# Kernel tuning notes

Hardware: AMD Instinct MI355X
Metric: run time of the kernel (lower is better)

The kernel has to match this reference:

```python
import jax, jax.numpy as jnp
import numpy as np

N = 8192       # nodes
E = 262144     # edges (avg degree 32)
F_IN, H, L = 512, 256, 64


def setup_inputs() -> dict:
    key = jax.random.key(0)
    ks = jax.random.split(key, 8)
    features = jax.random.normal(ks[0], (N, F_IN), dtype=jnp.float32)
    src = jax.random.randint(ks[1], (E,), 0, N)
    dst = jax.random.randint(ks[2], (E,), 0, N)
    # nn.Linear weights are [out_feats, in_feats]; scale ~ kaiming-ish small init
    W1 = jax.random.normal(ks[3], (H, F_IN), dtype=jnp.float32) * (1.0 / np.sqrt(F_IN))
    b1 = jnp.zeros((H,), dtype=jnp.float32)
    W2 = jax.random.normal(ks[4], (L, H), dtype=jnp.float32) * (1.0 / np.sqrt(H))
    b2 = jnp.zeros((L,), dtype=jnp.float32)
    W3 = jax.random.normal(ks[5], (L, H), dtype=jnp.float32) * (1.0 / np.sqrt(H))
    b3 = jnp.zeros((L,), dtype=jnp.float32)
    return {"features": features, "src": src, "dst": dst,
            "W1": W1, "b1": b1, "W2": W2, "b2": b2, "W3": W3, "b3": b3}


def _gcn_agg(h, src, dst):
    # DGL copy_src + sum: gather source node features along edges, scatter-sum to dst
    return jax.ops.segment_sum(h[src], dst, num_segments=N)  # [N, d]


def reference(features, src, dst, W1, b1, W2, b2, W3, b3):
    # GCN layer 1: aggregate then linear + relu  (dropout=0 -> identity)
    agg1 = _gcn_agg(features, src, dst)                 # [N, F_IN]
    hidden = jax.nn.relu(agg1 @ W1.T + b1)              # [N, H]
    # GCN layers 2 & 3 share the aggregated hidden (linear activation)
    agg2 = _gcn_agg(hidden, src, dst)                   # [N, H]
    mu = agg2 @ W2.T + b2                               # [N, L]
    logvar = agg2 @ W3.T + b3                           # [N, L]
    # eval-mode reparameterize: z = mu
    z = mu
    # inner-product decoder with sigmoid
    adj = jax.nn.sigmoid(z @ z.T)                       # [N, N]
    return adj, mu, logvar
```

## Files before the change

kernel.cpp:

```cpp
#include <hip/hip_runtime.h>
#include <hip/hip_bf16.h>

#define N_NODES 8192
#define N_EDGES 262144

typedef __attribute__((ext_vector_type(8))) short short8v;
typedef __attribute__((ext_vector_type(4))) float float4v;

static __device__ __forceinline__ unsigned short f2bf(float f) {
    unsigned u = __float_as_uint(f);
    unsigned r = (u + 0x7FFF + ((u >> 16) & 1)) >> 16;
    return (unsigned short)r;
}
static __device__ __forceinline__ float bf2f(unsigned short h) {
    return __uint_as_float(((unsigned)h) << 16);
}
static __device__ __forceinline__ short8v ld_cvt8(const float* p) {
    float4 lo = *(const float4*)p;
    float4 hi = *(const float4*)(p + 4);
    short8v r;
    r[0] = (short)f2bf(lo.x); r[1] = (short)f2bf(lo.y); r[2] = (short)f2bf(lo.z); r[3] = (short)f2bf(lo.w);
    r[4] = (short)f2bf(hi.x); r[5] = (short)f2bf(hi.y); r[6] = (short)f2bf(hi.z); r[7] = (short)f2bf(hi.w);
    return r;
}


__global__ __launch_bounds__(256) void hist_prep_kernel(const int* __restrict__ dst, int* __restrict__ deg,
                                                        const float* __restrict__ W1, const float* __restrict__ W2,
                                                        const float* __restrict__ W3,
                                                        unsigned short* __restrict__ W1b,
                                                        unsigned short* __restrict__ W23b) {
    int b = blockIdx.x;
    if (b < 1024) {
        int e = b * 256 + threadIdx.x;
        atomicAdd(&deg[dst[e]], 1);
        return;
    }
    int i4 = (b - 1024) * 1024 + threadIdx.x * 4;
    const float* srcp;
    unsigned short* dstp;
    int off;
    if (i4 < 131072)      { srcp = W1; dstp = W1b;          off = i4; }
    else if (i4 < 147456) { srcp = W2; dstp = W23b;         off = i4 - 131072; }
    else                  { srcp = W3; dstp = W23b + 16384; off = i4 - 147456; }
    float4 v = *(const float4*)&srcp[off];
    ushort4 o = {f2bf(v.x), f2bf(v.y), f2bf(v.z), f2bf(v.w)};
    *(ushort4*)&dstp[off] = o;
}

__global__ __launch_bounds__(256) void scatter_kernel(const int* __restrict__ src, const int* __restrict__ dst,
                                                      int* __restrict__ cur, int* __restrict__ csr) {
    int e = blockIdx.x * 256 + threadIdx.x;
    int d = dst[e];
    int p = atomicAdd(&cur[d], 1);
    csr[p] = src[e];
}


__global__ __launch_bounds__(256) void gemm1_scan_kernel(const float* __restrict__ X,
                                                         const unsigned short* __restrict__ W1b,
                                                         unsigned short* __restrict__ Y1b,
                                                         const int* __restrict__ deg,
                                                         int* __restrict__ offs, int* __restrict__ cur) {
    if (blockIdx.x == 256) {
        if (blockIdx.y != 0) return;
        __shared__ int wsum[4];
        int t = threadIdx.x, lane = t & 63, w = t >> 6;
        int v[32];
        int s = 0;
        const int4* dp = (const int4*)&deg[t * 32];
#pragma unroll
        for (int i = 0; i < 8; i++) {
            int4 x = dp[i];
            v[4*i] = x.x; v[4*i+1] = x.y; v[4*i+2] = x.z; v[4*i+3] = x.w;
            s += x.x + x.y + x.z + x.w;
        }
        int incl = s;
#pragma unroll
        for (int d = 1; d < 64; d <<= 1) {
            int u = __shfl_up(incl, d);
            if (lane >= d) incl += u;
        }
        if (lane == 63) wsum[w] = incl;
        __syncthreads();
        int base = 0;
#pragma unroll
        for (int i = 0; i < 4; i++) if (i < w) base += wsum[i];
        int ex = base + incl - s;
        int4* op = (int4*)&offs[t * 32];
        int4* cp = (int4*)&cur[t * 32];
#pragma unroll
        for (int i = 0; i < 8; i++) {
            int4 o;
            o.x = ex; ex += v[4*i];
            o.y = ex; ex += v[4*i+1];
            o.z = ex; ex += v[4*i+2];
            o.w = ex; ex += v[4*i+3];
            op[i] = o; cp[i] = o;
        }
        if (t == 255) offs[N_NODES] = ex;
        return;
    }
    const int tid = threadIdx.x;
    const int lane = tid & 63;
    const int w = tid >> 6;
    const int r = lane & 15, q = lane >> 4;
    const int m0 = blockIdx.x * 32;
    const int n0 = blockIdx.y * 128 + w * 32;
    const float* Ap = &X[q * 8];
    const unsigned short* Bp = &W1b[q * 8];
    float4v acc[2][2] = {};
    short8v a[2], b[2], an[2], bn[2];
#pragma unroll
    for (int i = 0; i < 2; i++) a[i] = ld_cvt8(&Ap[(size_t)(m0 + i * 16 + r) * 512]);
#pragma unroll
    for (int j = 0; j < 2; j++) b[j] = *(const short8v*)&Bp[(size_t)(n0 + j * 16 + r) * 512];
    for (int k = 32; k < 512; k += 32) {
#pragma unroll
        for (int i = 0; i < 2; i++) an[i] = ld_cvt8(&Ap[(size_t)(m0 + i * 16 + r) * 512 + k]);
#pragma unroll
        for (int j = 0; j < 2; j++) bn[j] = *(const short8v*)&Bp[(size_t)(n0 + j * 16 + r) * 512 + k];
#pragma unroll
        for (int i = 0; i < 2; i++)
#pragma unroll
            for (int j = 0; j < 2; j++)
                acc[i][j] = __builtin_amdgcn_mfma_f32_16x16x32_bf16(a[i], b[j], acc[i][j], 0, 0, 0);
#pragma unroll
        for (int i = 0; i < 2; i++) a[i] = an[i];
#pragma unroll
        for (int j = 0; j < 2; j++) b[j] = bn[j];
    }
#pragma unroll
    for (int i = 0; i < 2; i++)
#pragma unroll
        for (int j = 0; j < 2; j++)
            acc[i][j] = __builtin_amdgcn_mfma_f32_16x16x32_bf16(a[i], b[j], acc[i][j], 0, 0, 0);
#pragma unroll
    for (int i = 0; i < 2; i++)
#pragma unroll
        for (int j = 0; j < 2; j++) {
            int col = n0 + j * 16 + r;
#pragma unroll
            for (int t = 0; t < 4; t++) {
                int row = m0 + i * 16 + q * 4 + t;
                Y1b[(size_t)row * 256 + col] = f2bf(acc[i][j][t]);
            }
        }
}


__global__ __launch_bounds__(256) void agg_gemm2_kernel(const unsigned short* __restrict__ Yb,
                                                        const int* __restrict__ offs,
                                                        const int* __restrict__ csr,
                                                        const float* __restrict__ bias,
                                                        const unsigned short* __restrict__ W23b,
                                                        unsigned short* __restrict__ Zb) {
    __shared__ unsigned short Hs[16][264];
    const int w = threadIdx.x >> 6, lane = threadIdx.x & 63;
    const int nb = blockIdx.x * 16;
    float4 bv = *(const float4*)&bias[lane * 4];
    for (int nn = 0; nn < 4; nn++) {
        int node = nb + w * 4 + nn;
        int s = offs[node], e = offs[node + 1];
        float4 acc0 = {0.f, 0.f, 0.f, 0.f}, acc1 = {0.f, 0.f, 0.f, 0.f};
        int i = s;
        for (; i + 3 < e; i += 4) {
            int u0 = csr[i], u1 = csr[i + 1], u2 = csr[i + 2], u3 = csr[i + 3];
            ushort4 v0 = *(const ushort4*)&Yb[(size_t)u0 * 256 + lane * 4];
            ushort4 v1 = *(const ushort4*)&Yb[(size_t)u1 * 256 + lane * 4];
            ushort4 v2 = *(const ushort4*)&Yb[(size_t)u2 * 256 + lane * 4];
            ushort4 v3 = *(const ushort4*)&Yb[(size_t)u3 * 256 + lane * 4];
            acc0.x += bf2f(v0.x) + bf2f(v1.x); acc1.x += bf2f(v2.x) + bf2f(v3.x);
            acc0.y += bf2f(v0.y) + bf2f(v1.y); acc1.y += bf2f(v2.y) + bf2f(v3.y);
            acc0.z += bf2f(v0.z) + bf2f(v1.z); acc1.z += bf2f(v2.z) + bf2f(v3.z);
            acc0.w += bf2f(v0.w) + bf2f(v1.w); acc1.w += bf2f(v2.w) + bf2f(v3.w);
        }
        for (; i < e; i++) {
            int u = csr[i];
            ushort4 v = *(const ushort4*)&Yb[(size_t)u * 256 + lane * 4];
            acc0.x += bf2f(v.x); acc0.y += bf2f(v.y); acc0.z += bf2f(v.z); acc0.w += bf2f(v.w);
        }
        ushort4 o;
        o.x = f2bf(fmaxf(acc0.x + acc1.x + bv.x, 0.f));
        o.y = f2bf(fmaxf(acc0.y + acc1.y + bv.y, 0.f));
        o.z = f2bf(fmaxf(acc0.z + acc1.z + bv.z, 0.f));
        o.w = f2bf(fmaxf(acc0.w + acc1.w + bv.w, 0.f));
        *(ushort4*)&Hs[w * 4 + nn][lane * 4] = o;
    }
    __syncthreads();
    const int r = lane & 15, q = lane >> 4;
    const int jn0 = w * 32;
    float4v acc[2] = {};
#pragma unroll
    for (int k = 0; k < 256; k += 32) {
        short8v a  = *(const short8v*)&Hs[r][k + q * 8];
        short8v b0 = *(const short8v*)&W23b[(size_t)(jn0 + r) * 256 + k + q * 8];
        short8v b1 = *(const short8v*)&W23b[(size_t)(jn0 + 16 + r) * 256 + k + q * 8];
        acc[0] = __builtin_amdgcn_mfma_f32_16x16x32_bf16(a, b0, acc[0], 0, 0, 0);
        acc[1] = __builtin_amdgcn_mfma_f32_16x16x32_bf16(a, b1, acc[1], 0, 0, 0);
    }
#pragma unroll
    for (int j = 0; j < 2; j++)
#pragma unroll
        for (int t = 0; t < 4; t++)
            Zb[(size_t)(nb + q * 4 + t) * 128 + jn0 + j * 16 + r] = f2bf(acc[j][t]);
}


__global__ __launch_bounds__(256) void agg_split_kernel(const unsigned short* __restrict__ Zb,
                                                        const int* __restrict__ offs,
                                                        const int* __restrict__ csr, const float* __restrict__ b2,
                                                        const float* __restrict__ b3, float* __restrict__ mu,
                                                        float* __restrict__ lv, unsigned short* __restrict__ zb) {
    int node = blockIdx.x * 4 + (threadIdx.x >> 6);
    int lane = threadIdx.x & 63;
    int s = offs[node], e = offs[node + 1];
    float2 acc0 = {0.f, 0.f}, acc1 = {0.f, 0.f};
    int i = s;
    for (; i + 3 < e; i += 4) {
        int u0 = csr[i], u1 = csr[i + 1], u2 = csr[i + 2], u3 = csr[i + 3];
        ushort2 v0 = *(const ushort2*)&Zb[(size_t)u0 * 128 + lane * 2];
        ushort2 v1 = *(const ushort2*)&Zb[(size_t)u1 * 128 + lane * 2];
        ushort2 v2 = *(const ushort2*)&Zb[(size_t)u2 * 128 + lane * 2];
        ushort2 v3 = *(const ushort2*)&Zb[(size_t)u3 * 128 + lane * 2];
        acc0.x += bf2f(v0.x) + bf2f(v1.x); acc1.x += bf2f(v2.x) + bf2f(v3.x);
        acc0.y += bf2f(v0.y) + bf2f(v1.y); acc1.y += bf2f(v2.y) + bf2f(v3.y);
    }
    for (; i < e; i++) {
        int u = csr[i];
        ushort2 v = *(const ushort2*)&Zb[(size_t)u * 128 + lane * 2];
        acc0.x += bf2f(v.x); acc0.y += bf2f(v.y);
    }
    float2 acc = {acc0.x + acc1.x, acc0.y + acc1.y};
    int col = lane * 2;
    if (col < 64) {
        acc.x += b2[col]; acc.y += b2[col + 1];
        *(float2*)&mu[(size_t)node * 64 + col] = acc;
        ushort2 q = {f2bf(acc.x), f2bf(acc.y)};
        *(ushort2*)&zb[(size_t)node * 64 + col] = q;
    } else {
        col -= 64;
        acc.x += b3[col]; acc.y += b3[col + 1];
        *(float2*)&lv[(size_t)node * 64 + col] = acc;
    }
}


__global__ __launch_bounds__(256) void adj_mfma_sym_kernel(const unsigned short* __restrict__ zb,
                                                           float* __restrict__ out) {
    const int bx = blockIdx.x, by = blockIdx.y;
    if (by > bx) return;
    const int tid = threadIdx.x;
    const int lane = tid & 63;
    const int wid = tid >> 6;
    const int waveM = wid >> 1, waveN = wid & 1;
    const int m_base = bx * 128 + waveM * 64;
    const int n_base = by * 128 + waveN * 64;
    const int r = lane & 15;
    const int q = lane >> 4;

    short8v a[4][2], b[4][2];
#pragma unroll
    for (int i = 0; i < 4; i++)
#pragma unroll
        for (int s = 0; s < 2; s++) {
            a[i][s] = *(const short8v*)&zb[(size_t)(m_base + i * 16 + r) * 64 + s * 32 + q * 8];
            b[i][s] = *(const short8v*)&zb[(size_t)(n_base + i * 16 + r) * 64 + s * 32 + q * 8];
        }

    float4v acc[4][4] = {};
#pragma unroll
    for (int s = 0; s < 2; s++)
#pragma unroll
        for (int i = 0; i < 4; i++)
#pragma unroll
            for (int j = 0; j < 4; j++)
                acc[i][j] = __builtin_amdgcn_mfma_f32_16x16x32_bf16(a[i][s], b[j][s], acc[i][j], 0, 0, 0);

    const bool mirror = (bx != by);
#pragma unroll
    for (int i = 0; i < 4; i++)
#pragma unroll
        for (int j = 0; j < 4; j++) {
            int col = n_base + j * 16 + r;
            float4 vv;
#pragma unroll
            for (int t = 0; t < 4; t++) {
                int row = m_base + i * 16 + q * 4 + t;
                float v = 1.0f / (1.0f + __expf(-acc[i][j][t]));
                out[(size_t)row * N_NODES + col] = v;
                ((float*)&vv)[t] = v;
            }
            if (mirror) {
                *(float4*)&out[(size_t)col * N_NODES + m_base + i * 16 + q * 4] = vv;
            }
        }
}


extern "C" void kernel_launch(void* const* d_in, const int* in_sizes, int n_in,
                              void* d_out, int out_size, void* d_ws, size_t ws_size,
                              hipStream_t stream) {
    const float* X   = (const float*)d_in[0];
    const int*   src = (const int*)d_in[1];
    const int*   dst = (const int*)d_in[2];
    const float* W1  = (const float*)d_in[3];
    const float* b1  = (const float*)d_in[4];
    const float* W2  = (const float*)d_in[5];
    const float* b2  = (const float*)d_in[6];
    const float* W3  = (const float*)d_in[7];
    const float* b3  = (const float*)d_in[8];

    float* out    = (float*)d_out;
    float* adj    = out;
    float* mu_out = out + (size_t)N_NODES * N_NODES;
    float* lv_out = mu_out + (size_t)N_NODES * 64;

    char* ws = (char*)d_ws;
    size_t off = 0;
    auto alloc = [&](size_t bytes) -> void* {
        void* p = ws + off;
        off += (bytes + 1023) & ~(size_t)1023;
        return p;
    };
    int* deg            = (int*)alloc(N_NODES * 4);
    int* cur            = (int*)alloc(N_NODES * 4);
    int* offs           = (int*)alloc((N_NODES + 1) * 4);
    int* csr            = (int*)alloc(N_EDGES * 4);
    unsigned short* W1b = (unsigned short*)alloc(256 * 512 * 2);
    unsigned short* W23b= (unsigned short*)alloc(128 * 256 * 2);
    unsigned short* Y1b = (unsigned short*)alloc((size_t)N_NODES * 256 * 2);
    unsigned short* Zb  = (unsigned short*)alloc((size_t)N_NODES * 128 * 2);
    unsigned short* zb  = (unsigned short*)alloc((size_t)N_NODES * 64 * 2);

    hipMemsetAsync(deg, 0, N_NODES * sizeof(int), stream);
    hist_prep_kernel<<<1184, 256, 0, stream>>>(dst, deg, W1, W2, W3, W1b, W23b);
    gemm1_scan_kernel<<<dim3(257, 2), 256, 0, stream>>>(X, W1b, Y1b, deg, offs, cur);
    scatter_kernel<<<N_EDGES / 256, 256, 0, stream>>>(src, dst, cur, csr);
    agg_gemm2_kernel<<<N_NODES / 16, 256, 0, stream>>>(Y1b, offs, csr, b1, W23b, Zb);
    agg_split_kernel<<<N_NODES / 4, 256, 0, stream>>>(Zb, offs, csr, b2, b3, mu_out, lv_out, zb);
    adj_mfma_sym_kernel<<<dim3(64, 64), 256, 0, stream>>>(zb, adj);
}
```

Baseline: 429.9 us.

## Fuse degree histogram with GEMM1, drop weight pre-conversion, widen aggregation blocks

```diff
diff --git a/kernel.cpp b/kernel.cpp
--- a/kernel.cpp
+++ b/kernel.cpp
@@ -25,27 +25,103 @@
 }
 
 
-__global__ __launch_bounds__(256) void hist_prep_kernel(const int* __restrict__ dst, int* __restrict__ deg,
-                                                        const float* __restrict__ W1, const float* __restrict__ W2,
-                                                        const float* __restrict__ W3,
-                                                        unsigned short* __restrict__ W1b,
-                                                        unsigned short* __restrict__ W23b) {
-    int b = blockIdx.x;
+__global__ __launch_bounds__(256) void hist_gemm1_kernel(const int* __restrict__ dst, int* __restrict__ deg,
+                                                         const float* __restrict__ X,
+                                                         const float* __restrict__ W1,
+                                                         unsigned short* __restrict__ Y1b) {
+    const int b = blockIdx.x;
     if (b < 1024) {
         int e = b * 256 + threadIdx.x;
         atomicAdd(&deg[dst[e]], 1);
         return;
     }
-    int i4 = (b - 1024) * 1024 + threadIdx.x * 4;
-    const float* srcp;
-    unsigned short* dstp;
-    int off;
-    if (i4 < 131072)      { srcp = W1; dstp = W1b;          off = i4; }
-    else if (i4 < 147456) { srcp = W2; dstp = W23b;         off = i4 - 131072; }
-    else                  { srcp = W3; dstp = W23b + 16384; off = i4 - 147456; }
-    float4 v = *(const float4*)&srcp[off];
-    ushort4 o = {f2bf(v.x), f2bf(v.y), f2bf(v.z), f2bf(v.w)};
-    *(ushort4*)&dstp[off] = o;
+    const int g = b - 1024;
+    const int bx = g & 255, by = g >> 8;
+    const int tid = threadIdx.x;
+    const int lane = tid & 63;
+    const int w = tid >> 6;
+    const int r = lane & 15, q = lane >> 4;
+    const int m0 = bx * 32;
+    const int n0 = by * 128 + w * 32;
+    const float* Ap = &X[q * 8];
+    const float* Bp = &W1[q * 8];
+    float4v acc[2][2] = {};
+    short8v a[2], bb[2], an[2], bn[2];
+#pragma unroll
+    for (int i = 0; i < 2; i++) a[i] = ld_cvt8(&Ap[(size_t)(m0 + i * 16 + r) * 512]);
+#pragma unroll
+    for (int j = 0; j < 2; j++) bb[j] = ld_cvt8(&Bp[(size_t)(n0 + j * 16 + r) * 512]);
+    for (int k = 32; k < 512; k += 32) {
+#pragma unroll
+        for (int i = 0; i < 2; i++) an[i] = ld_cvt8(&Ap[(size_t)(m0 + i * 16 + r) * 512 + k]);
+#pragma unroll
+        for (int j = 0; j < 2; j++) bn[j] = ld_cvt8(&Bp[(size_t)(n0 + j * 16 + r) * 512 + k]);
+#pragma unroll
+        for (int i = 0; i < 2; i++)
+#pragma unroll
+            for (int j = 0; j < 2; j++)
+                acc[i][j] = __builtin_amdgcn_mfma_f32_16x16x32_bf16(a[i], bb[j], acc[i][j], 0, 0, 0);
+#pragma unroll
+        for (int i = 0; i < 2; i++) a[i] = an[i];
+#pragma unroll
+        for (int j = 0; j < 2; j++) bb[j] = bn[j];
+    }
+#pragma unroll
+    for (int i = 0; i < 2; i++)
+#pragma unroll
+        for (int j = 0; j < 2; j++)
+            acc[i][j] = __builtin_amdgcn_mfma_f32_16x16x32_bf16(a[i], bb[j], acc[i][j], 0, 0, 0);
+#pragma unroll
+    for (int i = 0; i < 2; i++)
+#pragma unroll
+        for (int j = 0; j < 2; j++) {
+            int col = n0 + j * 16 + r;
+#pragma unroll
+            for (int t = 0; t < 4; t++) {
+                int row = m0 + i * 16 + q * 4 + t;
+                Y1b[(size_t)row * 256 + col] = f2bf(acc[i][j][t]);
+            }
+        }
+}
+
+
+__global__ __launch_bounds__(256) void scan_kernel(const int* __restrict__ deg, int* __restrict__ offs,
+                                                   int* __restrict__ cur) {
+    __shared__ int wsum[4];
+    int t = threadIdx.x, lane = t & 63, w = t >> 6;
+    int v[32];
+    int s = 0;
+    const int4* dp = (const int4*)&deg[t * 32];
+#pragma unroll
+    for (int i = 0; i < 8; i++) {
+        int4 x = dp[i];
+        v[4*i] = x.x; v[4*i+1] = x.y; v[4*i+2] = x.z; v[4*i+3] = x.w;
+        s += x.x + x.y + x.z + x.w;
+    }
+    int incl = s;
+#pragma unroll
+    for (int d = 1; d < 64; d <<= 1) {
+        int u = __shfl_up(incl, d);
+        if (lane >= d) incl += u;
+    }
+    if (lane == 63) wsum[w] = incl;
+    __syncthreads();
+    int base = 0;
+#pragma unroll
+    for (int i = 0; i < 4; i++) if (i < w) base += wsum[i];
+    int ex = base + incl - s;
+    int4* op = (int4*)&offs[t * 32];
+    int4* cp = (int4*)&cur[t * 32];
+#pragma unroll
+    for (int i = 0; i < 8; i++) {
+        int4 o;
+        o.x = ex; ex += v[4*i];
+        o.y = ex; ex += v[4*i+1];
+        o.z = ex; ex += v[4*i+2];
+        o.w = ex; ex += v[4*i+3];
+        op[i] = o; cp[i] = o;
+    }
+    if (t == 255) offs[N_NODES] = ex;
 }
 
 __global__ __launch_bounds__(256) void scatter_kernel(const int* __restrict__ src, const int* __restrict__ dst,
@@ -57,110 +133,18 @@
 }
 
 
-__global__ __launch_bounds__(256) void gemm1_scan_kernel(const float* __restrict__ X,
-                                                         const unsigned short* __restrict__ W1b,
-                                                         unsigned short* __restrict__ Y1b,
-                                                         const int* __restrict__ deg,
-                                                         int* __restrict__ offs, int* __restrict__ cur) {
-    if (blockIdx.x == 256) {
-        if (blockIdx.y != 0) return;
-        __shared__ int wsum[4];
-        int t = threadIdx.x, lane = t & 63, w = t >> 6;
-        int v[32];
-        int s = 0;
-        const int4* dp = (const int4*)&deg[t * 32];
-#pragma unroll
-        for (int i = 0; i < 8; i++) {
-            int4 x = dp[i];
-            v[4*i] = x.x; v[4*i+1] = x.y; v[4*i+2] = x.z; v[4*i+3] = x.w;
-            s += x.x + x.y + x.z + x.w;
-        }
-        int incl = s;
-#pragma unroll
-        for (int d = 1; d < 64; d <<= 1) {
-            int u = __shfl_up(incl, d);
-            if (lane >= d) incl += u;
-        }
-        if (lane == 63) wsum[w] = incl;
-        __syncthreads();
-        int base = 0;
-#pragma unroll
-        for (int i = 0; i < 4; i++) if (i < w) base += wsum[i];
-        int ex = base + incl - s;
-        int4* op = (int4*)&offs[t * 32];
-        int4* cp = (int4*)&cur[t * 32];
-#pragma unroll
-        for (int i = 0; i < 8; i++) {
-            int4 o;
-            o.x = ex; ex += v[4*i];
-            o.y = ex; ex += v[4*i+1];
-            o.z = ex; ex += v[4*i+2];
-            o.w = ex; ex += v[4*i+3];
-            op[i] = o; cp[i] = o;
-        }
-        if (t == 255) offs[N_NODES] = ex;
-        return;
-    }
-    const int tid = threadIdx.x;
-    const int lane = tid & 63;
-    const int w = tid >> 6;
-    const int r = lane & 15, q = lane >> 4;
-    const int m0 = blockIdx.x * 32;
-    const int n0 = blockIdx.y * 128 + w * 32;
-    const float* Ap = &X[q * 8];
-    const unsigned short* Bp = &W1b[q * 8];
-    float4v acc[2][2] = {};
-    short8v a[2], b[2], an[2], bn[2];
-#pragma unroll
-    for (int i = 0; i < 2; i++) a[i] = ld_cvt8(&Ap[(size_t)(m0 + i * 16 + r) * 512]);
-#pragma unroll
-    for (int j = 0; j < 2; j++) b[j] = *(const short8v*)&Bp[(size_t)(n0 + j * 16 + r) * 512];
-    for (int k = 32; k < 512; k += 32) {
-#pragma unroll
-        for (int i = 0; i < 2; i++) an[i] = ld_cvt8(&Ap[(size_t)(m0 + i * 16 + r) * 512 + k]);
-#pragma unroll
-        for (int j = 0; j < 2; j++) bn[j] = *(const short8v*)&Bp[(size_t)(n0 + j * 16 + r) * 512 + k];
-#pragma unroll
-        for (int i = 0; i < 2; i++)
-#pragma unroll
-            for (int j = 0; j < 2; j++)
-                acc[i][j] = __builtin_amdgcn_mfma_f32_16x16x32_bf16(a[i], b[j], acc[i][j], 0, 0, 0);
-#pragma unroll
-        for (int i = 0; i < 2; i++) a[i] = an[i];
-#pragma unroll
-        for (int j = 0; j < 2; j++) b[j] = bn[j];
-    }
-#pragma unroll
-    for (int i = 0; i < 2; i++)
-#pragma unroll
-        for (int j = 0; j < 2; j++)
-            acc[i][j] = __builtin_amdgcn_mfma_f32_16x16x32_bf16(a[i], b[j], acc[i][j], 0, 0, 0);
-#pragma unroll
-    for (int i = 0; i < 2; i++)
-#pragma unroll
-        for (int j = 0; j < 2; j++) {
-            int col = n0 + j * 16 + r;
-#pragma unroll
-            for (int t = 0; t < 4; t++) {
-                int row = m0 + i * 16 + q * 4 + t;
-                Y1b[(size_t)row * 256 + col] = f2bf(acc[i][j][t]);
-            }
-        }
-}
-
-
-__global__ __launch_bounds__(256) void agg_gemm2_kernel(const unsigned short* __restrict__ Yb,
-                                                        const int* __restrict__ offs,
-                                                        const int* __restrict__ csr,
-                                                        const float* __restrict__ bias,
-                                                        const unsigned short* __restrict__ W23b,
-                                                        unsigned short* __restrict__ Zb) {
+__global__ __launch_bounds__(1024) void agg_gemm2_kernel(const unsigned short* __restrict__ Yb,
+                                                         const int* __restrict__ offs,
+                                                         const int* __restrict__ csr,
+                                                         const float* __restrict__ bias,
+                                                         const float* __restrict__ W2,
+                                                         const float* __restrict__ W3,
+                                                         unsigned short* __restrict__ Zb) {
     __shared__ unsigned short Hs[16][264];
     const int w = threadIdx.x >> 6, lane = threadIdx.x & 63;
     const int nb = blockIdx.x * 16;
-    float4 bv = *(const float4*)&bias[lane * 4];
-    for (int nn = 0; nn < 4; nn++) {
-        int node = nb + w * 4 + nn;
+    {
+        const int node = nb + w;
         int s = offs[node], e = offs[node + 1];
         float4 acc0 = {0.f, 0.f, 0.f, 0.f}, acc1 = {0.f, 0.f, 0.f, 0.f};
         int i = s;
@@ -180,30 +164,29 @@
             ushort4 v = *(const ushort4*)&Yb[(size_t)u * 256 + lane * 4];
             acc0.x += bf2f(v.x); acc0.y += bf2f(v.y); acc0.z += bf2f(v.z); acc0.w += bf2f(v.w);
         }
+        float4 bv = *(const float4*)&bias[lane * 4];
         ushort4 o;
         o.x = f2bf(fmaxf(acc0.x + acc1.x + bv.x, 0.f));
         o.y = f2bf(fmaxf(acc0.y + acc1.y + bv.y, 0.f));
         o.z = f2bf(fmaxf(acc0.z + acc1.z + bv.z, 0.f));
         o.w = f2bf(fmaxf(acc0.w + acc1.w + bv.w, 0.f));
-        *(ushort4*)&Hs[w * 4 + nn][lane * 4] = o;
+        *(ushort4*)&Hs[w][lane * 4] = o;
     }
     __syncthreads();
+    if (w >= 8) return;
     const int r = lane & 15, q = lane >> 4;
-    const int jn0 = w * 32;
-    float4v acc[2] = {};
+    const float* Wrow = (w < 4) ? &W2[(size_t)(w * 16 + r) * 256]
+                                : &W3[(size_t)((w - 4) * 16 + r) * 256];
+    float4v acc = {};
 #pragma unroll
     for (int k = 0; k < 256; k += 32) {
-        short8v a  = *(const short8v*)&Hs[r][k + q * 8];
-        short8v b0 = *(const short8v*)&W23b[(size_t)(jn0 + r) * 256 + k + q * 8];
-        short8v b1 = *(const short8v*)&W23b[(size_t)(jn0 + 16 + r) * 256 + k + q * 8];
-        acc[0] = __builtin_amdgcn_mfma_f32_16x16x32_bf16(a, b0, acc[0], 0, 0, 0);
-        acc[1] = __builtin_amdgcn_mfma_f32_16x16x32_bf16(a, b1, acc[1], 0, 0, 0);
-    }
-#pragma unroll
-    for (int j = 0; j < 2; j++)
-#pragma unroll
-        for (int t = 0; t < 4; t++)
-            Zb[(size_t)(nb + q * 4 + t) * 128 + jn0 + j * 16 + r] = f2bf(acc[j][t]);
+        short8v a = *(const short8v*)&Hs[r][k + q * 8];
+        short8v b = ld_cvt8(&Wrow[k + q * 8]);
+        acc = __builtin_amdgcn_mfma_f32_16x16x32_bf16(a, b, acc, 0, 0, 0);
+    }
+#pragma unroll
+    for (int t = 0; t < 4; t++)
+        Zb[(size_t)(nb + q * 4 + t) * 128 + w * 16 + r] = f2bf(acc[t]);
 }
 
 
@@ -327,17 +310,15 @@
     int* cur            = (int*)alloc(N_NODES * 4);
     int* offs           = (int*)alloc((N_NODES + 1) * 4);
     int* csr            = (int*)alloc(N_EDGES * 4);
-    unsigned short* W1b = (unsigned short*)alloc(256 * 512 * 2);
-    unsigned short* W23b= (unsigned short*)alloc(128 * 256 * 2);
     unsigned short* Y1b = (unsigned short*)alloc((size_t)N_NODES * 256 * 2);
     unsigned short* Zb  = (unsigned short*)alloc((size_t)N_NODES * 128 * 2);
     unsigned short* zb  = (unsigned short*)alloc((size_t)N_NODES * 64 * 2);
 
     hipMemsetAsync(deg, 0, N_NODES * sizeof(int), stream);
-    hist_prep_kernel<<<1184, 256, 0, stream>>>(dst, deg, W1, W2, W3, W1b, W23b);
-    gemm1_scan_kernel<<<dim3(257, 2), 256, 0, stream>>>(X, W1b, Y1b, deg, offs, cur);
+    hist_gemm1_kernel<<<1536, 256, 0, stream>>>(dst, deg, X, W1, Y1b);
+    scan_kernel<<<1, 256, 0, stream>>>(deg, offs, cur);
     scatter_kernel<<<N_EDGES / 256, 256, 0, stream>>>(src, dst, cur, csr);
-    agg_gemm2_kernel<<<N_NODES / 16, 256, 0, stream>>>(Y1b, offs, csr, b1, W23b, Zb);
+    agg_gemm2_kernel<<<N_NODES / 16, 1024, 0, stream>>>(Y1b, offs, csr, b1, W2, W3, Zb);
     agg_split_kernel<<<N_NODES / 4, 256, 0, stream>>>(Zb, offs, csr, b2, b3, mu_out, lv_out, zb);
     adj_mfma_sym_kernel<<<dim3(64, 64), 256, 0, stream>>>(zb, adj);
 }
```

Result: slower. 448.6 us (+4.3%).
